# Kernel optimization log

Measured on AMD Instinct MI355X. Metric: run time of the kernel, lower is better.

Reference implementation:

```python
import jax, jax.numpy as jnp
import numpy as np

GROUP_SIZE = 8  # channels per local region (64 channels -> 8 regions)
EPS_DEG = 0.001
NORM_EPS = 1e-12  # F.normalize eps
LEAKY_SLOPE = 0.2


def _build_mask(region_ids):
    # local adjacency: same region, i != j
    g = region_ids // GROUP_SIZE  # [C]
    same = g[:, None] == g[None, :]
    notself = ~jnp.eye(g.shape[0], dtype=bool)
    return same & notself  # [C, C] bool


def _build_normalized_adj(x, mask):
    # x: [B, N, D]; mask: [N, N] bool. self_loop=0, keep_neg=True.
    nrm = jnp.linalg.norm(x, axis=-1, keepdims=True)
    x_norm = x / jnp.maximum(nrm, NORM_EPS)
    S = jnp.einsum('bnd,bmd->bnm', x_norm, x_norm)  # cosine sims [B,N,N]
    S = jnp.where(mask[None, :, :], S, 0.0)
    S = 0.5 * (S + jnp.swapaxes(S, 1, 2))
    deg = jnp.maximum(S.sum(axis=-1), EPS_DEG)  # [B,N]
    dis = deg ** -0.5
    A = dis[:, :, None] * S * dis[:, None, :]  # diag scale instead of two matmuls
    return jnp.nan_to_num(A, nan=0.0, posinf=0.0, neginf=0.0)


def _gcn_layer(x, adj, W, b):
    h = jnp.einsum('bnm,bmd->bnd', adj, x)
    h = h @ W + b
    return jnp.where(h >= 0, h, LEAKY_SLOPE * h)


def setup_inputs() -> dict:
    key = jax.random.key(0)
    k = jax.random.split(key, 5)
    B, C, D = 4096, 64, 128
    x = jax.random.normal(k[0], (B, C, D), dtype=jnp.float32)
    region_ids = jnp.arange(C, dtype=jnp.int64 if jax.config.jax_enable_x64 else jnp.int32)
    s1 = (1.0 / D) ** 0.5
    W1 = jax.random.uniform(k[1], (D, D), jnp.float32, -s1, s1)
    b1 = jax.random.uniform(k[2], (D,), jnp.float32, -s1, s1)
    W2 = jax.random.uniform(k[3], (D, D), jnp.float32, -s1, s1)
    b2 = jax.random.uniform(k[4], (D,), jnp.float32, -s1, s1)
    return {"x": x, "region_ids": region_ids, "W1": W1, "b1": b1, "W2": W2, "b2": b2}


def reference(x, region_ids, W1, b1, W2, b2):
    mask = _build_mask(region_ids)
    adj = _build_normalized_adj(x, mask)
    x1 = _gcn_layer(x, adj, W1, b1)
    x1 = 0.5 * x1 + 0.5 * x
    x1 = _gcn_layer(x1, adj, W2, b2)
    return x1
```

## Files before the change

### kernel.cpp

```cpp
#include <hip/hip_runtime.h>
#include <hip/hip_bf16.h>


#define LDSP 132
#define HSP  136

typedef short bf16x8 __attribute__((ext_vector_type(8)));
typedef float f32x4  __attribute__((ext_vector_type(4)));

__device__ __forceinline__ float lrelu(float v) { return v >= 0.f ? v : 0.2f * v; }
__device__ __forceinline__ ushort f2bf(float f) {
    return __bfloat16_as_ushort(__float2bfloat16(f));
}
__device__ __forceinline__ float bf2f(ushort u) {
    return __uint_as_float(((unsigned)u) << 16);
}

#define PIDX(i, j) ((j) * ((j) + 1) / 2 + (i))

__global__ void prep_wt_hi(const float* __restrict__ W1, const float* __restrict__ W2,
                           ushort* __restrict__ w1h, ushort* __restrict__ w2h) {
    int idx = blockIdx.x * 256 + threadIdx.x;
    int n = idx >> 7, k = idx & 127;
    w1h[idx] = f2bf(W1[k * 128 + n]);
    w2h[idx] = f2bf(W2[k * 128 + n]);
}

__global__ void prep_wt_hl(const float* __restrict__ W1, const float* __restrict__ W2,
                           ushort* __restrict__ w1h, ushort* __restrict__ w1l,
                           ushort* __restrict__ w2h, ushort* __restrict__ w2l) {
    int idx = blockIdx.x * 256 + threadIdx.x;
    int n = idx >> 7, k = idx & 127;
    float a = W1[k * 128 + n];
    ushort ah = f2bf(a);
    w1h[idx] = ah;
    w1l[idx] = f2bf(a - bf2f(ah));
    float b = W2[k * 128 + n];
    ushort bh = f2bf(b);
    w2h[idx] = bh;
    w2l[idx] = f2bf(b - bf2f(bh));
}

__device__ __forceinline__ void spmm_phase(
    float (*src)[LDSP], ushort (*hh)[HSP], float (*As)[8], int t)
{
    const int g  = t >> 5;
    const int h  = (t >> 4) & 1;
    const int cp = t & 15;
    const int r0 = g * 8 + h * 4;

    f32x4 a0[4], a1[4];
#pragma unroll
    for (int ri = 0; ri < 4; ++ri) {
        a0[ri] = *(const f32x4*)&As[r0 + ri][0];
        a1[ri] = *(const f32x4*)&As[r0 + ri][4];
    }
    f32x4 acc[4][2];
#pragma unroll
    for (int ri = 0; ri < 4; ++ri)
#pragma unroll
        for (int q = 0; q < 2; ++q)
            acc[ri][q] = (f32x4){0.f, 0.f, 0.f, 0.f};

#pragma unroll
    for (int j = 0; j < 8; ++j) {
#pragma unroll
        for (int q = 0; q < 2; ++q) {
            const int f4 = cp + 16 * q;
            f32x4 xv = *(const f32x4*)&src[g * 8 + j][f4 * 4];
#pragma unroll
            for (int ri = 0; ri < 4; ++ri) {
                const float aj = (j < 4) ? a0[ri][j] : a1[ri][j - 4];
                acc[ri][q] += xv * aj;
            }
        }
    }
#pragma unroll
    for (int ri = 0; ri < 4; ++ri)
#pragma unroll
        for (int q = 0; q < 2; ++q) {
            ushort4 oh;
#pragma unroll
            for (int e = 0; e < 4; ++e)
                ((ushort*)&oh)[e] = f2bf(acc[ri][q][e]);
            *(ushort4*)&hh[r0 + ri][(cp + 16 * q) * 4] = oh;
        }
}

template <bool FINAL, bool WSPLIT>
__device__ __forceinline__ void mfma_dense(
    float (*xs)[LDSP], ushort (*hh)[HSP],
    const ushort* __restrict__ wth, const ushort* __restrict__ wtl,
    const float* __restrict__ bias, float* __restrict__ outp, int t)
{
    const int w = t >> 6, lane = t & 63;
    const int lr = lane & 15;
    const int lk = lane >> 4;
    const int colbase = w * 32;

    f32x4 acc[4][2];
#pragma unroll
    for (int m = 0; m < 4; ++m)
#pragma unroll
        for (int n = 0; n < 2; ++n)
            acc[m][n] = (f32x4){0.f, 0.f, 0.f, 0.f};

#pragma unroll
    for (int kt = 0; kt < 4; ++kt) {
        const int kk = kt * 32 + lk * 8;
        bf16x8 bh[2], bl[2];
#pragma unroll
        for (int n = 0; n < 2; ++n) {
            const size_t off = (size_t)(colbase + n * 16 + lr) * 128 + kk;
            bh[n] = *(const bf16x8*)(wth + off);
            if (WSPLIT) bl[n] = *(const bf16x8*)(wtl + off);
        }
        bf16x8 ah[4];
#pragma unroll
        for (int m = 0; m < 4; ++m)
            ah[m] = *(const bf16x8*)&hh[m * 16 + lr][kk];
#pragma unroll
        for (int m = 0; m < 4; ++m)
#pragma unroll
            for (int n = 0; n < 2; ++n) {
                acc[m][n] = __builtin_amdgcn_mfma_f32_16x16x32_bf16(
                    ah[m], bh[n], acc[m][n], 0, 0, 0);
                if (WSPLIT)
                    acc[m][n] = __builtin_amdgcn_mfma_f32_16x16x32_bf16(
                        ah[m], bl[n], acc[m][n], 0, 0, 0);
            }
    }

#pragma unroll
    for (int m = 0; m < 4; ++m) {
#pragma unroll
        for (int n = 0; n < 2; ++n) {
            const int ocol = colbase + n * 16 + lr;
            const float bb = bias[ocol];
#pragma unroll
            for (int j = 0; j < 4; ++j) {
                const int orow = m * 16 + lk * 4 + j;
                float v = lrelu(acc[m][n][j] + bb);
                if (FINAL) {
                    outp[orow * 128 + ocol] = v;
                } else {
                    xs[orow][ocol] = 0.5f * v + 0.5f * xs[orow][ocol];
                }
            }
        }
    }
}

template <bool WSPLIT>
__global__ __launch_bounds__(256, 3) void gcn_fused(
    const float* __restrict__ x,
    const ushort* __restrict__ w1h, const ushort* __restrict__ w1l,
    const float* __restrict__ b1,
    const ushort* __restrict__ w2h, const ushort* __restrict__ w2l,
    const float* __restrict__ b2,
    float* __restrict__ out)
{
    __shared__ __align__(16) float  xs[64][LDSP];
    __shared__ __align__(16) ushort hh[64][HSP];
    __shared__ __align__(16) float  As[64][8];

    float* scratch = (float*)&hh[0][0];
    float (*dots4)[8][40] = (float(*)[8][40])scratch;
    float* invn = scratch + 4 * 8 * 40;
    float* dis  = invn + 64;

    const int t = threadIdx.x;
    const size_t boff = (size_t)blockIdx.x * (64 * 128);

    {
        const float4* src = (const float4*)(x + boff);
#pragma unroll
        for (int i = 0; i < 8; ++i) {
            int f = t + i * 256;
            int r = f >> 5;
            int c = (f & 31) * 4;
            *(float4*)&xs[r][c] = src[f];
        }
    }
    __syncthreads();

    {
        const int qh = t >> 6;
        const int g  = (t >> 3) & 7;
        const int ks = t & 7;
        const int f4 = qh * 8 + ks;
        f32x4 rv[8];
#pragma unroll
        for (int j = 0; j < 8; ++j)
            rv[j] = *(const f32x4*)&xs[g * 8 + j][f4 * 4];
        float s[36];
        {
            int p = 0;
#pragma unroll
            for (int j = 0; j < 8; ++j)
#pragma unroll
                for (int i = 0; i <= j; ++i) {
                    s[p] = rv[i][0] * rv[j][0] + rv[i][1] * rv[j][1]
                         + rv[i][2] * rv[j][2] + rv[i][3] * rv[j][3];
                    ++p;
                }
        }
#pragma unroll
        for (int d = 1; d < 8; d <<= 1)
#pragma unroll
            for (int p = 0; p < 36; ++p)
                s[p] += __shfl_xor(s[p], d, 64);
        if (ks == 0) {
#pragma unroll
            for (int p = 0; p < 36; ++p)
                dots4[qh][g][p] = s[p];
        }
    }
    __syncthreads();

    float cs[8];
    float ii_r = 0.f, di_r = 0.f;
    if (t < 64) {
        int g = t >> 3, i = t & 7;
        int pd = PIDX(i, i);
        float n2 = dots4[0][g][pd] + dots4[1][g][pd]
                 + dots4[2][g][pd] + dots4[3][g][pd];
        ii_r = 1.0f / fmaxf(sqrtf(n2), 1e-12f);
        invn[t] = ii_r;
    }
    __syncthreads();

    if (t < 64) {
        int g = t >> 3, i = t & 7;
        float deg = 0.f;
#pragma unroll
        for (int j = 0; j < 8; ++j) {
            int p = (i <= j) ? PIDX(i, j) : PIDX(j, i);
            float d = dots4[0][g][p] + dots4[1][g][p]
                    + dots4[2][g][p] + dots4[3][g][p];
            cs[j] = d * ii_r * invn[g * 8 + j];
            if (j != i) deg += cs[j];
        }
        di_r = rsqrtf(fmaxf(deg, 0.001f));
        dis[t] = di_r;
    }
    __syncthreads();

    if (t < 64) {
        int g = t >> 3, i = t & 7;
#pragma unroll
        for (int j = 0; j < 8; ++j) {
            float a = (j == i) ? 0.f : cs[j] * di_r * dis[g * 8 + j];
            As[t][j] = a;
        }
    }
    __syncthreads();

    spmm_phase(xs, hh, As, t);
    __syncthreads();
    mfma_dense<false, WSPLIT>(xs, hh, w1h, w1l, b1, nullptr, t);
    __syncthreads();

    spmm_phase(xs, hh, As, t);
    __syncthreads();
    mfma_dense<true, WSPLIT>(xs, hh, w2h, w2l, b2, out + boff, t);
}

extern "C" void kernel_launch(void* const* d_in, const int* in_sizes, int n_in,
                              void* d_out, int out_size, void* d_ws, size_t ws_size,
                              hipStream_t stream) {
    const float* x  = (const float*)d_in[0];
    const float* W1 = (const float*)d_in[2];
    const float* b1 = (const float*)d_in[3];
    const float* W2 = (const float*)d_in[4];
    const float* b2 = (const float*)d_in[5];
    float* out = (float*)d_out;

    const int Bn = in_sizes[0] / (64 * 128);
    const size_t MAT = 128 * 128;

    if (ws_size >= 4 * MAT * sizeof(ushort)) {
        ushort* w1h = (ushort*)d_ws;
        ushort* w1l = w1h + MAT;
        ushort* w2h = w1l + MAT;
        ushort* w2l = w2h + MAT;
        prep_wt_hl<<<64, 256, 0, stream>>>(W1, W2, w1h, w1l, w2h, w2l);
        gcn_fused<true><<<Bn, 256, 0, stream>>>(x, w1h, w1l, b1, w2h, w2l, b2, out);
    } else {
        ushort* w1h = (ushort*)d_ws;
        ushort* w2h = w1h + MAT;
        prep_wt_hi<<<64, 256, 0, stream>>>(W1, W2, w1h, w2h);
        gcn_fused<false><<<Bn, 256, 0, stream>>>(x, w1h, w1h, b1, w2h, w2h, b2, out);
    }
}
```

Before: 105.1 us.

## Split each batch across two blocks of 32 channels to raise occupancy

The 8-channel groups are independent, so each block now handles half a batch (4 groups, 32 rows) and the grid doubles. Shared-memory footprint per block halves and launch bounds go from 3 to 4 blocks per CU, aiming for more resident waves to hide global-memory latency. The SpMM and MFMA phases are re-mapped to the smaller tile. In exchange, every block reloads the weight matrices (more L2 traffic), and the dot-product phase now computes redundant duplicate groups.

```diff
diff --git a/kernel.cpp b/kernel.cpp
--- a/kernel.cpp
+++ b/kernel.cpp
@@ -44,10 +44,10 @@
 __device__ __forceinline__ void spmm_phase(
     float (*src)[LDSP], ushort (*hh)[HSP], float (*As)[8], int t)
 {
-    const int g  = t >> 5;
-    const int h  = (t >> 4) & 1;
-    const int cp = t & 15;
-    const int r0 = g * 8 + h * 4;
+    const int rq = t >> 5;
+    const int cp = t & 31;
+    const int r0 = rq * 4;
+    const int gb = r0 & ~7;
 
     f32x4 a0[4], a1[4];
 #pragma unroll
@@ -55,36 +55,28 @@
         a0[ri] = *(const f32x4*)&As[r0 + ri][0];
         a1[ri] = *(const f32x4*)&As[r0 + ri][4];
     }
-    f32x4 acc[4][2];
+    f32x4 acc[4];
 #pragma unroll
     for (int ri = 0; ri < 4; ++ri)
-#pragma unroll
-        for (int q = 0; q < 2; ++q)
-            acc[ri][q] = (f32x4){0.f, 0.f, 0.f, 0.f};
+        acc[ri] = (f32x4){0.f, 0.f, 0.f, 0.f};
 
 #pragma unroll
     for (int j = 0; j < 8; ++j) {
-#pragma unroll
-        for (int q = 0; q < 2; ++q) {
-            const int f4 = cp + 16 * q;
-            f32x4 xv = *(const f32x4*)&src[g * 8 + j][f4 * 4];
-#pragma unroll
-            for (int ri = 0; ri < 4; ++ri) {
-                const float aj = (j < 4) ? a0[ri][j] : a1[ri][j - 4];
-                acc[ri][q] += xv * aj;
-            }
-        }
-    }
-#pragma unroll
-    for (int ri = 0; ri < 4; ++ri)
-#pragma unroll
-        for (int q = 0; q < 2; ++q) {
-            ushort4 oh;
-#pragma unroll
-            for (int e = 0; e < 4; ++e)
-                ((ushort*)&oh)[e] = f2bf(acc[ri][q][e]);
-            *(ushort4*)&hh[r0 + ri][(cp + 16 * q) * 4] = oh;
-        }
+        f32x4 xv = *(const f32x4*)&src[gb + j][cp * 4];
+#pragma unroll
+        for (int ri = 0; ri < 4; ++ri) {
+            const float aj = (j < 4) ? a0[ri][j] : a1[ri][j - 4];
+            acc[ri] += xv * aj;
+        }
+    }
+#pragma unroll
+    for (int ri = 0; ri < 4; ++ri) {
+        ushort4 oh;
+#pragma unroll
+        for (int e = 0; e < 4; ++e)
+            ((ushort*)&oh)[e] = f2bf(acc[ri][e]);
+        *(ushort4*)&hh[r0 + ri][cp * 4] = oh;
+    }
 }
 
 template <bool FINAL, bool WSPLIT>
@@ -98,9 +90,9 @@
     const int lk = lane >> 4;
     const int colbase = w * 32;
 
-    f32x4 acc[4][2];
-#pragma unroll
-    for (int m = 0; m < 4; ++m)
+    f32x4 acc[2][2];
+#pragma unroll
+    for (int m = 0; m < 2; ++m)
 #pragma unroll
         for (int n = 0; n < 2; ++n)
             acc[m][n] = (f32x4){0.f, 0.f, 0.f, 0.f};
@@ -115,12 +107,12 @@
             bh[n] = *(const bf16x8*)(wth + off);
             if (WSPLIT) bl[n] = *(const bf16x8*)(wtl + off);
         }
-        bf16x8 ah[4];
-#pragma unroll
-        for (int m = 0; m < 4; ++m)
+        bf16x8 ah[2];
+#pragma unroll
+        for (int m = 0; m < 2; ++m)
             ah[m] = *(const bf16x8*)&hh[m * 16 + lr][kk];
 #pragma unroll
-        for (int m = 0; m < 4; ++m)
+        for (int m = 0; m < 2; ++m)
 #pragma unroll
             for (int n = 0; n < 2; ++n) {
                 acc[m][n] = __builtin_amdgcn_mfma_f32_16x16x32_bf16(
@@ -132,7 +124,7 @@
     }
 
 #pragma unroll
-    for (int m = 0; m < 4; ++m) {
+    for (int m = 0; m < 2; ++m) {
 #pragma unroll
         for (int n = 0; n < 2; ++n) {
             const int ocol = colbase + n * 16 + lr;
@@ -152,7 +144,7 @@
 }
 
 template <bool WSPLIT>
-__global__ __launch_bounds__(256, 3) void gcn_fused(
+__global__ __launch_bounds__(256, 4) void gcn_fused(
     const float* __restrict__ x,
     const ushort* __restrict__ w1h, const ushort* __restrict__ w1l,
     const float* __restrict__ b1,
@@ -160,22 +152,24 @@
     const float* __restrict__ b2,
     float* __restrict__ out)
 {
-    __shared__ __align__(16) float  xs[64][LDSP];
-    __shared__ __align__(16) ushort hh[64][HSP];
-    __shared__ __align__(16) float  As[64][8];
+    __shared__ __align__(16) float  xs[32][LDSP];
+    __shared__ __align__(16) ushort hh[32][HSP];
+    __shared__ __align__(16) float  As[32][8];
 
     float* scratch = (float*)&hh[0][0];
     float (*dots4)[8][40] = (float(*)[8][40])scratch;
     float* invn = scratch + 4 * 8 * 40;
-    float* dis  = invn + 64;
+    float* dis  = invn + 32;
 
     const int t = threadIdx.x;
-    const size_t boff = (size_t)blockIdx.x * (64 * 128);
+    const int batch = blockIdx.x >> 1;
+    const int half  = blockIdx.x & 1;
+    const size_t boff = (size_t)batch * (64 * 128) + (size_t)half * (32 * 128);
 
     {
         const float4* src = (const float4*)(x + boff);
 #pragma unroll
-        for (int i = 0; i < 8; ++i) {
+        for (int i = 0; i < 4; ++i) {
             int f = t + i * 256;
             int r = f >> 5;
             int c = (f & 31) * 4;
@@ -192,7 +186,7 @@
         f32x4 rv[8];
 #pragma unroll
         for (int j = 0; j < 8; ++j)
-            rv[j] = *(const f32x4*)&xs[g * 8 + j][f4 * 4];
+            rv[j] = *(const f32x4*)&xs[(g & 3) * 8 + j][f4 * 4];
         float s[36];
         {
             int p = 0;
@@ -220,7 +214,7 @@
 
     float cs[8];
     float ii_r = 0.f, di_r = 0.f;
-    if (t < 64) {
+    if (t < 32) {
         int g = t >> 3, i = t & 7;
         int pd = PIDX(i, i);
         float n2 = dots4[0][g][pd] + dots4[1][g][pd]
@@ -230,7 +224,7 @@
     }
     __syncthreads();
 
-    if (t < 64) {
+    if (t < 32) {
         int g = t >> 3, i = t & 7;
         float deg = 0.f;
 #pragma unroll
@@ -246,7 +240,7 @@
     }
     __syncthreads();
 
-    if (t < 64) {
+    if (t < 32) {
         int g = t >> 3, i = t & 7;
 #pragma unroll
         for (int j = 0; j < 8; ++j) {
@@ -285,11 +279,11 @@
         ushort* w2h = w1l + MAT;
         ushort* w2l = w2h + MAT;
         prep_wt_hl<<<64, 256, 0, stream>>>(W1, W2, w1h, w1l, w2h, w2l);
-        gcn_fused<true><<<Bn, 256, 0, stream>>>(x, w1h, w1l, b1, w2h, w2l, b2, out);
+        gcn_fused<true><<<Bn * 2, 256, 0, stream>>>(x, w1h, w1l, b1, w2h, w2l, b2, out);
     } else {
         ushort* w1h = (ushort*)d_ws;
         ushort* w2h = w1h + MAT;
         prep_wt_hi<<<64, 256, 0, stream>>>(W1, W2, w1h, w2h);
-        gcn_fused<false><<<Bn, 256, 0, stream>>>(x, w1h, w1h, b1, w2h, w2h, b2, out);
-    }
-}
+        gcn_fused<false><<<Bn * 2, 256, 0, stream>>>(x, w1h, w1h, b1, w2h, w2h, b2, out);
+    }
+}
```

After: 145.4 us. +38.4%, slower.

## Reorder GCN layers to apply the dense MFMA before the block-diagonal adjacency

Applied to the files above, without the earlier changes.

Uses associativity to compute (X·W) first with MFMA on a bf16 copy of the input, then applies the 8x8 block-diagonal adjacency in registers through a cross-lane shuffle, instead of running a separate LDS-based SpMM phase before each matmul. The bf16 copy of x is built during the initial load. The Gram-reduction layout changes so each group is reduced in a single 32-lane pass, which drops the cross-quarter partial sums and their scratch buffer. This removes two LDS SpMM passes and some barriers. In exchange it adds shuffles and register pressure, and it rounds the raw input to bf16 before the first layer, which may change accuracy.

```diff
diff --git a/kernel.cpp b/kernel.cpp
--- a/kernel.cpp
+++ b/kernel.cpp
@@ -41,62 +41,16 @@
     w2l[idx] = f2bf(b - bf2f(bh));
 }
 
-__device__ __forceinline__ void spmm_phase(
-    float (*src)[LDSP], ushort (*hh)[HSP], float (*As)[8], int t)
+template <bool WSPLIT>
+__device__ __forceinline__ void mfma_layer(
+    ushort (*xb)[HSP], float (*As)[8],
+    const ushort* __restrict__ wth, const ushort* __restrict__ wtl,
+    int t, f32x4 (&res)[4][2])
 {
-    const int g  = t >> 5;
-    const int h  = (t >> 4) & 1;
-    const int cp = t & 15;
-    const int r0 = g * 8 + h * 4;
-
-    f32x4 a0[4], a1[4];
-#pragma unroll
-    for (int ri = 0; ri < 4; ++ri) {
-        a0[ri] = *(const f32x4*)&As[r0 + ri][0];
-        a1[ri] = *(const f32x4*)&As[r0 + ri][4];
-    }
-    f32x4 acc[4][2];
-#pragma unroll
-    for (int ri = 0; ri < 4; ++ri)
-#pragma unroll
-        for (int q = 0; q < 2; ++q)
-            acc[ri][q] = (f32x4){0.f, 0.f, 0.f, 0.f};
-
-#pragma unroll
-    for (int j = 0; j < 8; ++j) {
-#pragma unroll
-        for (int q = 0; q < 2; ++q) {
-            const int f4 = cp + 16 * q;
-            f32x4 xv = *(const f32x4*)&src[g * 8 + j][f4 * 4];
-#pragma unroll
-            for (int ri = 0; ri < 4; ++ri) {
-                const float aj = (j < 4) ? a0[ri][j] : a1[ri][j - 4];
-                acc[ri][q] += xv * aj;
-            }
-        }
-    }
-#pragma unroll
-    for (int ri = 0; ri < 4; ++ri)
-#pragma unroll
-        for (int q = 0; q < 2; ++q) {
-            ushort4 oh;
-#pragma unroll
-            for (int e = 0; e < 4; ++e)
-                ((ushort*)&oh)[e] = f2bf(acc[ri][q][e]);
-            *(ushort4*)&hh[r0 + ri][(cp + 16 * q) * 4] = oh;
-        }
-}
-
-template <bool FINAL, bool WSPLIT>
-__device__ __forceinline__ void mfma_dense(
-    float (*xs)[LDSP], ushort (*hh)[HSP],
-    const ushort* __restrict__ wth, const ushort* __restrict__ wtl,
-    const float* __restrict__ bias, float* __restrict__ outp, int t)
-{
-    const int w = t >> 6, lane = t & 63;
+    const int lane = t & 63;
     const int lr = lane & 15;
     const int lk = lane >> 4;
-    const int colbase = w * 32;
+    const int colbase = (t >> 6) * 32;
 
     f32x4 acc[4][2];
 #pragma unroll
@@ -118,7 +72,7 @@
         bf16x8 ah[4];
 #pragma unroll
         for (int m = 0; m < 4; ++m)
-            ah[m] = *(const bf16x8*)&hh[m * 16 + lr][kk];
+            ah[m] = *(const bf16x8*)&xb[m * 16 + lr][kk];
 #pragma unroll
         for (int m = 0; m < 4; ++m)
 #pragma unroll
@@ -131,21 +85,37 @@
             }
     }
 
+    const bool odd = (lk & 1) != 0;
 #pragma unroll
     for (int m = 0; m < 4; ++m) {
-#pragma unroll
-        for (int n = 0; n < 2; ++n) {
-            const int ocol = colbase + n * 16 + lr;
-            const float bb = bias[ocol];
-#pragma unroll
-            for (int j = 0; j < 4; ++j) {
-                const int orow = m * 16 + lk * 4 + j;
-                float v = lrelu(acc[m][n][j] + bb);
-                if (FINAL) {
-                    outp[orow * 128 + ocol] = v;
-                } else {
-                    xs[orow][ocol] = 0.5f * v + 0.5f * xs[orow][ocol];
-                }
+        f32x4 a0[4], a1[4];
+#pragma unroll
+        for (int j = 0; j < 4; ++j) {
+            const int r = m * 16 + lk * 4 + j;
+            a0[j] = *(const f32x4*)&As[r][0];
+            a1[j] = *(const f32x4*)&As[r][4];
+        }
+#pragma unroll
+        for (int n = 0; n < 2; ++n) {
+            float own[4], prt[4];
+#pragma unroll
+            for (int j = 0; j < 4; ++j) {
+                own[j] = acc[m][n][j];
+                prt[j] = __shfl_xor(acc[m][n][j], 16, 64);
+            }
+            float ylo[4], yhi[4];
+#pragma unroll
+            for (int j = 0; j < 4; ++j) {
+                ylo[j] = odd ? prt[j] : own[j];
+                yhi[j] = odd ? own[j] : prt[j];
+            }
+#pragma unroll
+            for (int j = 0; j < 4; ++j) {
+                res[m][n][j] =
+                      a0[j][0] * ylo[0] + a0[j][1] * ylo[1]
+                    + a0[j][2] * ylo[2] + a0[j][3] * ylo[3]
+                    + a1[j][0] * yhi[0] + a1[j][1] * yhi[1]
+                    + a1[j][2] * yhi[2] + a1[j][3] * yhi[3];
             }
         }
     }
@@ -161,16 +131,20 @@
     float* __restrict__ out)
 {
     __shared__ __align__(16) float  xs[64][LDSP];
-    __shared__ __align__(16) ushort hh[64][HSP];
+    __shared__ __align__(16) ushort xb[64][HSP];
     __shared__ __align__(16) float  As[64][8];
-
-    float* scratch = (float*)&hh[0][0];
-    float (*dots4)[8][40] = (float(*)[8][40])scratch;
-    float* invn = scratch + 4 * 8 * 40;
-    float* dis  = invn + 64;
+    __shared__ float invn[64];
+    __shared__ float dis[64];
+
+    float* dotsF = (float*)&As[0][0];
 
     const int t = threadIdx.x;
     const size_t boff = (size_t)blockIdx.x * (64 * 128);
+
+    const int lane = t & 63;
+    const int lr = lane & 15;
+    const int lk = lane >> 4;
+    const int colbase = (t >> 6) * 32;
 
     {
         const float4* src = (const float4*)(x + boff);
@@ -179,16 +153,19 @@
             int f = t + i * 256;
             int r = f >> 5;
             int c = (f & 31) * 4;
-            *(float4*)&xs[r][c] = src[f];
+            float4 v = src[f];
+            *(float4*)&xs[r][c] = v;
+            ushort4 vb;
+            vb.x = f2bf(v.x); vb.y = f2bf(v.y);
+            vb.z = f2bf(v.z); vb.w = f2bf(v.w);
+            *(ushort4*)&xb[r][c] = vb;
         }
     }
     __syncthreads();
 
     {
-        const int qh = t >> 6;
-        const int g  = (t >> 3) & 7;
-        const int ks = t & 7;
-        const int f4 = qh * 8 + ks;
+        const int g  = t >> 5;
+        const int f4 = t & 31;
         f32x4 rv[8];
 #pragma unroll
         for (int j = 0; j < 8; ++j)
@@ -206,14 +183,14 @@
                 }
         }
 #pragma unroll
-        for (int d = 1; d < 8; d <<= 1)
+        for (int d = 1; d < 32; d <<= 1)
 #pragma unroll
             for (int p = 0; p < 36; ++p)
                 s[p] += __shfl_xor(s[p], d, 64);
-        if (ks == 0) {
+        if (f4 == 0) {
 #pragma unroll
             for (int p = 0; p < 36; ++p)
-                dots4[qh][g][p] = s[p];
+                dotsF[g * 40 + p] = s[p];
         }
     }
     __syncthreads();
@@ -222,9 +199,7 @@
     float ii_r = 0.f, di_r = 0.f;
     if (t < 64) {
         int g = t >> 3, i = t & 7;
-        int pd = PIDX(i, i);
-        float n2 = dots4[0][g][pd] + dots4[1][g][pd]
-                 + dots4[2][g][pd] + dots4[3][g][pd];
+        float n2 = dotsF[g * 40 + PIDX(i, i)];
         ii_r = 1.0f / fmaxf(sqrtf(n2), 1e-12f);
         invn[t] = ii_r;
     }
@@ -236,9 +211,7 @@
 #pragma unroll
         for (int j = 0; j < 8; ++j) {
             int p = (i <= j) ? PIDX(i, j) : PIDX(j, i);
-            float d = dots4[0][g][p] + dots4[1][g][p]
-                    + dots4[2][g][p] + dots4[3][g][p];
-            cs[j] = d * ii_r * invn[g * 8 + j];
+            cs[j] = dotsF[g * 40 + p] * ii_r * invn[g * 8 + j];
             if (j != i) deg += cs[j];
         }
         di_r = rsqrtf(fmaxf(deg, 0.001f));
@@ -256,14 +229,53 @@
     }
     __syncthreads();
 
-    spmm_phase(xs, hh, As, t);
-    __syncthreads();
-    mfma_dense<false, WSPLIT>(xs, hh, w1h, w1l, b1, nullptr, t);
-    __syncthreads();
-
-    spmm_phase(xs, hh, As, t);
-    __syncthreads();
-    mfma_dense<true, WSPLIT>(xs, hh, w2h, w2l, b2, out + boff, t);
+    f32x4 r1[4][2];
+    mfma_layer<WSPLIT>(xb, As, w1h, w1l, t, r1);
+
+    ushort x1b[4][2][4];
+#pragma unroll
+    for (int m = 0; m < 4; ++m)
+#pragma unroll
+        for (int n = 0; n < 2; ++n) {
+            const int ocol = colbase + n * 16 + lr;
+            const float bb = b1[ocol];
+#pragma unroll
+            for (int j = 0; j < 4; ++j) {
+                const int orow = m * 16 + lk * 4 + j;
+                float v = lrelu(r1[m][n][j] + bb);
+                v = 0.5f * v + 0.5f * xs[orow][ocol];
+                x1b[m][n][j] = f2bf(v);
+            }
+        }
+    __syncthreads();
+
+#pragma unroll
+    for (int m = 0; m < 4; ++m)
+#pragma unroll
+        for (int n = 0; n < 2; ++n) {
+            const int ocol = colbase + n * 16 + lr;
+#pragma unroll
+            for (int j = 0; j < 4; ++j)
+                xb[m * 16 + lk * 4 + j][ocol] = x1b[m][n][j];
+        }
+    __syncthreads();
+
+    f32x4 r2[4][2];
+    mfma_layer<WSPLIT>(xb, As, w2h, w2l, t, r2);
+
+    float* outp = out + boff;
+#pragma unroll
+    for (int m = 0; m < 4; ++m)
+#pragma unroll
+        for (int n = 0; n < 2; ++n) {
+            const int ocol = colbase + n * 16 + lr;
+            const float bb = b2[ocol];
+#pragma unroll
+            for (int j = 0; j < 4; ++j) {
+                const int orow = m * 16 + lk * 4 + j;
+                outp[orow * 128 + ocol] = lrelu(r2[m][n][j] + bb);
+            }
+        }
 }
 
 extern "C" void kernel_launch(void* const* d_in, const int* in_sizes, int n_in,
```

Measured after the change: 140.2 us. +33.4%, slower.
